# Optimization experiments

Hardware: AMD Instinct MI355X
Metric: run time of the kernel (lower is better)

The kernel has to match this reference:

```python
import jax, jax.numpy as jnp
import numpy as np

N_NODES = 50000
N_EDGES = 600000
IN_DIM = 128
OUT_DIM = 128
EPS = 1e-5


def setup_inputs() -> dict:
    key = jax.random.key(0)
    k1, k2, k3 = jax.random.split(key, 3)
    h = jax.random.normal(k1, (N_NODES, IN_DIM), dtype=jnp.float32)
    edge_index = jax.random.randint(k2, (2, N_EDGES), 0, N_NODES, dtype=jnp.int64)
    ln_gamma = jnp.ones((IN_DIM,), dtype=jnp.float32)
    ln_beta = jnp.zeros((IN_DIM,), dtype=jnp.float32)
    W = jax.random.normal(k3, (OUT_DIM, 2 * IN_DIM), dtype=jnp.float32) * (1.0 / np.sqrt(2 * IN_DIM))
    b = jnp.zeros((OUT_DIM,), dtype=jnp.float32)
    return {"h": h, "edge_index": edge_index, "ln_gamma": ln_gamma,
            "ln_beta": ln_beta, "W": W, "b": b}


def _layernorm(x, gamma, beta):
    mu = jnp.mean(x, axis=-1, keepdims=True)
    var = jnp.mean(jnp.square(x - mu), axis=-1, keepdims=True)
    return (x - mu) * jax.lax.rsqrt(var + EPS) * gamma + beta


def reference(h, edge_index, ln_gamma, ln_beta, W, b):
    src, dst = edge_index[0], edge_index[1]
    n = h.shape[0]
    # LayerNorm
    hn = _layernorm(h, ln_gamma, ln_beta)  # [N, D]
    # Degrees (DGL norm='both' clamps to min 1)
    ones = jnp.ones((src.shape[0],), dtype=h.dtype)
    deg_out = jnp.clip(jax.ops.segment_sum(ones, src, num_segments=n), 1.0)
    deg_in = jnp.clip(jax.ops.segment_sum(ones, dst, num_segments=n), 1.0)
    inv_sqrt_out = jax.lax.rsqrt(deg_out)  # [N]
    inv_sqrt_in = jax.lax.rsqrt(deg_in)    # [N]
    # SpMM: message = D_in^{-1/2} A D_out^{-1/2} hn
    msg_src = hn * inv_sqrt_out[:, None]                 # scale at source
    gathered = msg_src[src]                              # [E, D] irregular gather
    agg = jax.ops.segment_sum(gathered, dst, num_segments=n)  # [N, D]
    message = agg * inv_sqrt_in[:, None]
    # Concat + Linear (dropout is identity in eval)
    cat = jnp.concatenate([hn, message], axis=1)  # [N, 2D]
    return cat @ W.T + b
```

## Files before the change

kernel.cpp:

```cpp
#include <hip/hip_runtime.h>
#include <stdint.h>

#define N_NODES 50000
#define N_EDGES 600000
#define D       128
#define EPS     1e-5f
#define HG      64
#define NWORDS  25000

typedef __attribute__((ext_vector_type(8))) short bf16x8;
typedef __attribute__((ext_vector_type(4))) float f32x4;

__device__ __forceinline__ unsigned short f2bf(float x) {
    unsigned int u = __float_as_uint(x);
    return (unsigned short)((u + 0x7fffu + ((u >> 16) & 1u)) >> 16);
}

__device__ __forceinline__ int load_idx(const void* e, long long i, int is64) {
    return is64 ? (int)((const long long*)e)[i] : ((const int*)e)[i];
}

__device__ __forceinline__ int block_detect64(const unsigned int* eraw, int* sflag) {
    if (threadIdx.x < 64) {
        unsigned long long nz = __ballot(eraw[2 * threadIdx.x + 1] != 0u);
        if (threadIdx.x == 0) *sflag = (nz == 0ull) ? 1 : 0;
    }
    __syncthreads();
    return *sflag;
}

__global__ __launch_bounds__(1024) void hist_kernel(const unsigned int* __restrict__ eraw,
                                                    unsigned int* __restrict__ partials) {
    __shared__ unsigned int lhist[NWORDS];
    __shared__ int sflag;
    int t = threadIdx.x;
    int which = blockIdx.x >= HG;
    int b     = blockIdx.x & (HG - 1);
    for (int i = t; i < NWORDS; i += 1024) lhist[i] = 0u;
    int is64 = block_detect64(eraw, &sflag);
    const int per = N_EDGES / HG;
    int lo = b * per, hi = lo + per;
    long long base = which ? (long long)N_EDGES : 0ll;
    for (int i = lo + t; i < hi; i += 1024) {
        int v = load_idx(eraw, base + i, is64);
        atomicAdd(&lhist[v >> 1], (v & 1) ? (1u << 16) : 1u);
    }
    __syncthreads();
    unsigned int* dst = partials + (size_t)blockIdx.x * NWORDS;
    for (int i = t; i < NWORDS; i += 1024) dst[i] = lhist[i];
}

__global__ __launch_bounds__(256) void deg_reduce(const unsigned int* __restrict__ partials,
                                                  unsigned int* __restrict__ deg_in,
                                                  float* __restrict__ inv_out,
                                                  float* __restrict__ inv_in) {
    int w = blockIdx.x * 256 + threadIdx.x;
    if (w >= NWORDS) return;
    unsigned int o0 = 0, o1 = 0, d0 = 0, d1 = 0;
    for (int b = 0; b < HG; ++b) {
        unsigned int p = partials[(size_t)b * NWORDS + w];
        o0 += p & 0xffffu; o1 += p >> 16;
    }
    for (int b = 0; b < HG; ++b) {
        unsigned int p = partials[(size_t)(HG + b) * NWORDS + w];
        d0 += p & 0xffffu; d1 += p >> 16;
    }
    deg_in[2 * w]     = d0;
    deg_in[2 * w + 1] = d1;
    inv_out[2 * w]     = rsqrtf((float)(o0 > 1u ? o0 : 1u));
    inv_out[2 * w + 1] = rsqrtf((float)(o1 > 1u ? o1 : 1u));
    inv_in[2 * w]      = rsqrtf((float)(d0 > 1u ? d0 : 1u));
    inv_in[2 * w + 1]  = rsqrtf((float)(d1 > 1u ? d1 : 1u));
}

__global__ __launch_bounds__(1024) void scan1(const unsigned int* __restrict__ deg,
                                              unsigned int* __restrict__ row_start,
                                              unsigned int* __restrict__ partials) {
    __shared__ unsigned int wsum[16];
    int t = threadIdx.x, lane = t & 63, w = t >> 6;
    int i = blockIdx.x * 1024 + t;
    unsigned int v = (i < N_NODES) ? deg[i] : 0u;
    unsigned int x = v;
    #pragma unroll
    for (int off = 1; off < 64; off <<= 1) {
        unsigned int y = __shfl_up(x, off, 64);
        if (lane >= off) x += y;
    }
    if (lane == 63) wsum[w] = x;
    __syncthreads();
    if (w == 0) {
        unsigned int s = (lane < 16) ? wsum[lane] : 0u;
        #pragma unroll
        for (int off = 1; off < 16; off <<= 1) {
            unsigned int y = __shfl_up(s, off, 64);
            if (lane >= off) s += y;
        }
        if (lane < 16) wsum[lane] = s;
    }
    __syncthreads();
    unsigned int excl = (w ? wsum[w - 1] : 0u) + x - v;
    if (i < N_NODES) row_start[i] = excl;
    if (t == 1023) partials[blockIdx.x] = wsum[15];
}

__global__ __launch_bounds__(1024) void scan2(const unsigned int* __restrict__ partials,
                                              unsigned int* __restrict__ row_start) {
    __shared__ unsigned int soff;
    int t = threadIdx.x, b = blockIdx.x;
    if (t < 64) {
        unsigned int p = (t < b) ? partials[t] : 0u;
        #pragma unroll
        for (int off = 32; off; off >>= 1) p += __shfl_xor(p, off, 64);
        if (t == 0) soff = p;
    }
    __syncthreads();
    int i = b * 1024 + t;
    if (i < N_NODES) row_start[i] += soff;
    if (b == 0 && t == 0) row_start[N_NODES] = N_EDGES;
}

__global__ __launch_bounds__(256) void prefix_kernel(const unsigned int* __restrict__ partials,
                                                     const unsigned int* __restrict__ row_start,
                                                     unsigned int* __restrict__ pre) {
    int w = blockIdx.x * 256 + threadIdx.x;
    if (w >= NWORDS) return;
    unsigned int run0 = row_start[2 * w], run1 = row_start[2 * w + 1];
    for (int b = 0; b < HG; ++b) {
        pre[(size_t)b * N_NODES + 2 * w]     = run0;
        pre[(size_t)b * N_NODES + 2 * w + 1] = run1;
        unsigned int p = partials[(size_t)(HG + b) * NWORDS + w];
        run0 += p & 0xffffu; run1 += p >> 16;
    }
}

__global__ __launch_bounds__(1024) void fill_kernel(const unsigned int* __restrict__ eraw,
                                                    const unsigned int* __restrict__ pre,
                                                    unsigned int* __restrict__ csr_src) {
    __shared__ unsigned int lcur[NWORDS];
    __shared__ int sflag;
    int t = threadIdx.x, b = blockIdx.x;
    for (int i = t; i < NWORDS; i += 1024) lcur[i] = 0u;
    int is64 = block_detect64(eraw, &sflag);
    const int per = N_EDGES / HG;
    int lo = b * per, hi = lo + per;
    const unsigned int* preb = pre + (size_t)b * N_NODES;
    for (int i = lo + t; i < hi; i += 1024) {
        int s = load_idx(eraw, i, is64);
        int d = load_idx(eraw, (long long)N_EDGES + i, is64);
        unsigned int old = atomicAdd(&lcur[d >> 1], (d & 1) ? (1u << 16) : 1u);
        unsigned int pl = (d & 1) ? (old >> 16) : (old & 0xffffu);
        csr_src[preb[d] + pl] = (unsigned int)s;
    }
}

__global__ __launch_bounds__(256) void ln_kernel(const float2* __restrict__ h2,
                                                 const float2* __restrict__ g2,
                                                 const float2* __restrict__ b2,
                                                 unsigned int* __restrict__ hnb) {
    int wid  = threadIdx.x >> 6;
    int lane = threadIdx.x & 63;
    int row  = blockIdx.x * 4 + wid;
    if (row >= N_NODES) return;
    float2 v = h2[(size_t)row * 64 + lane];
    float s  = v.x + v.y;
    float ss = v.x * v.x + v.y * v.y;
    #pragma unroll
    for (int off = 32; off; off >>= 1) {
        s  += __shfl_xor(s,  off, 64);
        ss += __shfl_xor(ss, off, 64);
    }
    float mu  = s * (1.0f / D);
    float var = ss * (1.0f / D) - mu * mu;
    float rs  = rsqrtf(var + EPS);
    float2 g = g2[lane], b = b2[lane];
    float y0 = (v.x - mu) * rs * g.x + b.x;
    float y1 = (v.y - mu) * rs * g.y + b.y;
    hnb[(size_t)row * 64 + lane] = (unsigned int)f2bf(y0) | ((unsigned int)f2bf(y1) << 16);
}

__global__ __launch_bounds__(256) void cast_W(const float2* __restrict__ W2,
                                              unsigned int* __restrict__ Wb) {
    int i = blockIdx.x * 256 + threadIdx.x;
    if (i < 128 * 128) {
        float2 w = W2[i];
        Wb[i] = (unsigned int)f2bf(w.x) | ((unsigned int)f2bf(w.y) << 16);
    }
}

__global__ __launch_bounds__(256) void agg_kernel(const unsigned int* __restrict__ hnb,
                                                  const float* __restrict__ inv_out,
                                                  const float* __restrict__ inv_in,
                                                  const unsigned int* __restrict__ row_start,
                                                  const unsigned int* __restrict__ csr_src,
                                                  unsigned int* __restrict__ aggb) {
    int wid  = threadIdx.x >> 6;
    int lane = threadIdx.x & 63;
    int row  = blockIdx.x * 4 + wid;
    if (row >= N_NODES) return;
    int g = lane >> 4, gl = lane & 15;
    unsigned int e0 = row_start[row], e1 = row_start[row + 1];
    float acc[8];
    #pragma unroll
    for (int j = 0; j < 8; ++j) acc[j] = 0.0f;

    unsigned int e = e0;
    while (e < e1) {
        unsigned int cnt = e1 - e;
        if (cnt > 64u) cnt = 64u;
        int sl = (lane < (int)cnt) ? (int)csr_src[e + lane] : 0;
        int nit = ((int)cnt + 3) >> 2;
        for (int it = 0; it < nit; ++it) {
            int idx = it * 4 + g;
            int s = __shfl(sl, idx, 64);
            if (idx < (int)cnt) {
                float sc = inv_out[s];
                uint4 v = *(const uint4*)(hnb + (size_t)s * 64 + gl * 4);
                acc[0] = fmaf(__uint_as_float(v.x << 16),          sc, acc[0]);
                acc[1] = fmaf(__uint_as_float(v.x & 0xffff0000u),  sc, acc[1]);
                acc[2] = fmaf(__uint_as_float(v.y << 16),          sc, acc[2]);
                acc[3] = fmaf(__uint_as_float(v.y & 0xffff0000u),  sc, acc[3]);
                acc[4] = fmaf(__uint_as_float(v.z << 16),          sc, acc[4]);
                acc[5] = fmaf(__uint_as_float(v.z & 0xffff0000u),  sc, acc[5]);
                acc[6] = fmaf(__uint_as_float(v.w << 16),          sc, acc[6]);
                acc[7] = fmaf(__uint_as_float(v.w & 0xffff0000u),  sc, acc[7]);
            }
        }
        e += cnt;
    }
    #pragma unroll
    for (int j = 0; j < 8; ++j) {
        acc[j] += __shfl_xor(acc[j], 16, 64);
        acc[j] += __shfl_xor(acc[j], 32, 64);
    }
    if (g == 0) {
        float ii = inv_in[row];
        uint4 o;
        o.x = (unsigned int)f2bf(acc[0] * ii) | ((unsigned int)f2bf(acc[1] * ii) << 16);
        o.y = (unsigned int)f2bf(acc[2] * ii) | ((unsigned int)f2bf(acc[3] * ii) << 16);
        o.z = (unsigned int)f2bf(acc[4] * ii) | ((unsigned int)f2bf(acc[5] * ii) << 16);
        o.w = (unsigned int)f2bf(acc[6] * ii) | ((unsigned int)f2bf(acc[7] * ii) << 16);
        *(uint4*)(aggb + (size_t)row * 64 + gl * 4) = o;
    }
}

__global__ __launch_bounds__(256) void gemm_kernel(const unsigned short* __restrict__ hnb,
                                                   const unsigned short* __restrict__ aggb,
                                                   const unsigned short* __restrict__ Wb,
                                                   const float* __restrict__ bias,
                                                   float* __restrict__ out) {
    __shared__ unsigned short wlds[128 * 264];
    int t = threadIdx.x;
    {
        int j = t >> 1, half = t & 1;
        const uint4* src = (const uint4*)(Wb + (size_t)j * 256 + half * 128);
        uint4* dst = (uint4*)(wlds + j * 264 + half * 128);
        #pragma unroll
        for (int i = 0; i < 16; ++i) dst[i] = src[i];
    }
    __syncthreads();

    int w = t >> 6, lane = t & 63;
    int rbase = blockIdx.x * 64 + w * 16;
    if (rbase >= N_NODES) return;
    int lrow = lane & 15, lhi = lane >> 4;

    bf16x8 a[8];
    const unsigned short* hrow = hnb + (size_t)(rbase + lrow) * 128 + lhi * 8;
    const unsigned short* arow = aggb + (size_t)(rbase + lrow) * 128 + lhi * 8;
    #pragma unroll
    for (int kc = 0; kc < 4; ++kc) a[kc]     = *(const bf16x8*)(hrow + kc * 32);
    #pragma unroll
    for (int kc = 0; kc < 4; ++kc) a[4 + kc] = *(const bf16x8*)(arow + kc * 32);

    f32x4 acc[8];
    #pragma unroll
    for (int ct = 0; ct < 8; ++ct) acc[ct] = (f32x4){0.f, 0.f, 0.f, 0.f};

    #pragma unroll
    for (int ct = 0; ct < 8; ++ct) {
        const unsigned short* bb = wlds + (ct * 16 + lrow) * 264 + lhi * 8;
        #pragma unroll
        for (int kc = 0; kc < 8; ++kc) {
            bf16x8 bfrag = *(const bf16x8*)(bb + kc * 32);
            acc[ct] = __builtin_amdgcn_mfma_f32_16x16x32_bf16(a[kc], bfrag, acc[ct], 0, 0, 0);
        }
    }

    #pragma unroll
    for (int ct = 0; ct < 8; ++ct) {
        int col = ct * 16 + lrow;
        float bv = bias[col];
        #pragma unroll
        for (int i = 0; i < 4; ++i) {
            int row = rbase + lhi * 4 + i;
            out[(size_t)row * 128 + col] = acc[ct][i] + bv;
        }
    }
}

extern "C" void kernel_launch(void* const* d_in, const int* in_sizes, int n_in,
                              void* d_out, int out_size, void* d_ws, size_t ws_size,
                              hipStream_t stream) {
    const float* h     = (const float*)d_in[0];
    const unsigned int* eraw = (const unsigned int*)d_in[1];
    const float* gamma = (const float*)d_in[2];
    const float* beta  = (const float*)d_in[3];
    const float* W     = (const float*)d_in[4];
    const float* bias  = (const float*)d_in[5];
    float* out = (float*)d_out;

    char* ws = (char*)d_ws;
    size_t off = 0;
    auto alloc = [&](size_t bytes) { size_t o = off; off += (bytes + 255) & ~(size_t)255; return o; };
    unsigned int* hpart     = (unsigned int*)(ws + alloc((size_t)2 * HG * NWORDS * 4));
    unsigned int* pre       = (unsigned int*)(ws + alloc((size_t)HG * N_NODES * 4));
    unsigned int* deg_in    = (unsigned int*)(ws + alloc((size_t)N_NODES * 4));
    float*        inv_out   = (float*)(ws + alloc((size_t)N_NODES * 4));
    float*        inv_in    = (float*)(ws + alloc((size_t)N_NODES * 4));
    unsigned int* row_start = (unsigned int*)(ws + alloc((size_t)(N_NODES + 1) * 4));
    unsigned int* spart     = (unsigned int*)(ws + alloc(64 * 4));
    unsigned int* Wb        = (unsigned int*)(ws + alloc((size_t)128 * 256 * 2));
    unsigned int* csr_src   = (unsigned int*)(ws + alloc((size_t)N_EDGES * 4));
    unsigned int* hnb       = (unsigned int*)(ws + alloc((size_t)N_NODES * D * 2));
    unsigned int* aggb      = (unsigned int*)(ws + alloc((size_t)N_NODES * D * 2));

    hist_kernel<<<2 * HG, 1024, 0, stream>>>(eraw, hpart);
    ln_kernel<<<(N_NODES + 3) / 4, 256, 0, stream>>>((const float2*)h, (const float2*)gamma,
                                                     (const float2*)beta, hnb);
    deg_reduce<<<(NWORDS + 255) / 256, 256, 0, stream>>>(hpart, deg_in, inv_out, inv_in);
    scan1<<<(N_NODES + 1023) / 1024, 1024, 0, stream>>>(deg_in, row_start, spart);
    scan2<<<(N_NODES + 1023) / 1024, 1024, 0, stream>>>(spart, row_start);
    prefix_kernel<<<(NWORDS + 255) / 256, 256, 0, stream>>>(hpart, row_start, pre);
    cast_W<<<64, 256, 0, stream>>>((const float2*)W, Wb);
    fill_kernel<<<HG, 1024, 0, stream>>>(eraw, pre, csr_src);
    agg_kernel<<<(N_NODES + 3) / 4, 256, 0, stream>>>(hnb, inv_out, inv_in, row_start,
                                                      csr_src, aggb);
    gemm_kernel<<<(N_NODES + 63) / 64, 256, 0, stream>>>((const unsigned short*)hnb,
                                                         (const unsigned short*)aggb,
                                                         (const unsigned short*)Wb,
                                                         bias, out);
}
```

Measured before the change: 110.1 us.

## Fuse degree reduce into scan, prefix into scan2, W cast into hist; widen agg gather

Merges the degree reduction into the first scan kernel, the per-block prefix computation into the second scan kernel, and the W bf16 cast into the histogram kernel. Together these cut the launch count from ten to seven and drop the deg_in buffer. The aggregation kernel now processes 8 edges per wave iteration, with each lane loading two 16-byte chunks and keeping 16 accumulators, instead of 4 edges per iteration. The fused scan reads partials per node rather than per word, which doubles those reads. The wider aggregation raises register pressure.

```diff
diff --git a/kernel.cpp b/kernel.cpp
--- a/kernel.cpp
+++ b/kernel.cpp
@@ -30,7 +30,9 @@
 }
 
 __global__ __launch_bounds__(1024) void hist_kernel(const unsigned int* __restrict__ eraw,
-                                                    unsigned int* __restrict__ partials) {
+                                                    unsigned int* __restrict__ partials,
+                                                    const float2* __restrict__ W2,
+                                                    unsigned int* __restrict__ Wb) {
     __shared__ unsigned int lhist[NWORDS];
     __shared__ int sflag;
     int t = threadIdx.x;
@@ -48,38 +50,35 @@
     __syncthreads();
     unsigned int* dst = partials + (size_t)blockIdx.x * NWORDS;
     for (int i = t; i < NWORDS; i += 1024) dst[i] = lhist[i];
-}
-
-__global__ __launch_bounds__(256) void deg_reduce(const unsigned int* __restrict__ partials,
-                                                  unsigned int* __restrict__ deg_in,
-                                                  float* __restrict__ inv_out,
-                                                  float* __restrict__ inv_in) {
-    int w = blockIdx.x * 256 + threadIdx.x;
-    if (w >= NWORDS) return;
-    unsigned int o0 = 0, o1 = 0, d0 = 0, d1 = 0;
-    for (int b = 0; b < HG; ++b) {
-        unsigned int p = partials[(size_t)b * NWORDS + w];
-        o0 += p & 0xffffu; o1 += p >> 16;
-    }
-    for (int b = 0; b < HG; ++b) {
-        unsigned int p = partials[(size_t)(HG + b) * NWORDS + w];
-        d0 += p & 0xffffu; d1 += p >> 16;
-    }
-    deg_in[2 * w]     = d0;
-    deg_in[2 * w + 1] = d1;
-    inv_out[2 * w]     = rsqrtf((float)(o0 > 1u ? o0 : 1u));
-    inv_out[2 * w + 1] = rsqrtf((float)(o1 > 1u ? o1 : 1u));
-    inv_in[2 * w]      = rsqrtf((float)(d0 > 1u ? d0 : 1u));
-    inv_in[2 * w + 1]  = rsqrtf((float)(d1 > 1u ? d1 : 1u));
-}
-
-__global__ __launch_bounds__(1024) void scan1(const unsigned int* __restrict__ deg,
-                                              unsigned int* __restrict__ row_start,
-                                              unsigned int* __restrict__ partials) {
+    if (blockIdx.x == 0) {
+        for (int i = t; i < 128 * 128; i += 1024) {
+            float2 w = W2[i];
+            Wb[i] = (unsigned int)f2bf(w.x) | ((unsigned int)f2bf(w.y) << 16);
+        }
+    }
+}
+
+__global__ __launch_bounds__(1024) void scan1r(const unsigned int* __restrict__ partials,
+                                               float* __restrict__ inv_out,
+                                               float* __restrict__ inv_in,
+                                               unsigned int* __restrict__ row_start,
+                                               unsigned int* __restrict__ spart) {
     __shared__ unsigned int wsum[16];
     int t = threadIdx.x, lane = t & 63, w = t >> 6;
     int i = blockIdx.x * 1024 + t;
-    unsigned int v = (i < N_NODES) ? deg[i] : 0u;
+    unsigned int od = 0, dd = 0;
+    if (i < N_NODES) {
+        int word = i >> 1, hi = i & 1;
+        for (int b = 0; b < HG; ++b) {
+            unsigned int ps = partials[(size_t)b * NWORDS + word];
+            unsigned int pd = partials[(size_t)(HG + b) * NWORDS + word];
+            od += hi ? (ps >> 16) : (ps & 0xffffu);
+            dd += hi ? (pd >> 16) : (pd & 0xffffu);
+        }
+        inv_out[i] = rsqrtf((float)(od > 1u ? od : 1u));
+        inv_in[i]  = rsqrtf((float)(dd > 1u ? dd : 1u));
+    }
+    unsigned int v = (i < N_NODES) ? dd : 0u;
     unsigned int x = v;
     #pragma unroll
     for (int off = 1; off < 64; off <<= 1) {
@@ -100,36 +99,40 @@
     __syncthreads();
     unsigned int excl = (w ? wsum[w - 1] : 0u) + x - v;
     if (i < N_NODES) row_start[i] = excl;
-    if (t == 1023) partials[blockIdx.x] = wsum[15];
-}
-
-__global__ __launch_bounds__(1024) void scan2(const unsigned int* __restrict__ partials,
-                                              unsigned int* __restrict__ row_start) {
-    __shared__ unsigned int soff;
+    if (t == 1023) spart[blockIdx.x] = wsum[15];
+}
+
+__global__ __launch_bounds__(1024) void scan2p(const unsigned int* __restrict__ partials,
+                                               const unsigned int* __restrict__ spart,
+                                               unsigned int* __restrict__ row_start,
+                                               unsigned int* __restrict__ pre) {
+    __shared__ unsigned int soff_s;
     int t = threadIdx.x, b = blockIdx.x;
     if (t < 64) {
-        unsigned int p = (t < b) ? partials[t] : 0u;
+        unsigned int p = (t < b) ? spart[t] : 0u;
         #pragma unroll
         for (int off = 32; off; off >>= 1) p += __shfl_xor(p, off, 64);
-        if (t == 0) soff = p;
-    }
-    __syncthreads();
+        if (t == 0) soff_s = p;
+    }
+    __syncthreads();
+    unsigned int soff = soff_s;
     int i = b * 1024 + t;
     if (i < N_NODES) row_start[i] += soff;
     if (b == 0 && t == 0) row_start[N_NODES] = N_EDGES;
-}
-
-__global__ __launch_bounds__(256) void prefix_kernel(const unsigned int* __restrict__ partials,
-                                                     const unsigned int* __restrict__ row_start,
-                                                     unsigned int* __restrict__ pre) {
-    int w = blockIdx.x * 256 + threadIdx.x;
-    if (w >= NWORDS) return;
-    unsigned int run0 = row_start[2 * w], run1 = row_start[2 * w + 1];
-    for (int b = 0; b < HG; ++b) {
-        pre[(size_t)b * N_NODES + 2 * w]     = run0;
-        pre[(size_t)b * N_NODES + 2 * w + 1] = run1;
-        unsigned int p = partials[(size_t)(HG + b) * NWORDS + w];
-        run0 += p & 0xffffu; run1 += p >> 16;
+    __syncthreads();
+    if (t < 512) {
+        int w2 = b * 512 + t;
+        if (w2 < NWORDS) {
+            unsigned int run0 = row_start[2 * w2];
+            unsigned int run1 = row_start[2 * w2 + 1];
+            for (int bb = 0; bb < HG; ++bb) {
+                pre[(size_t)bb * N_NODES + 2 * w2]     = run0;
+                pre[(size_t)bb * N_NODES + 2 * w2 + 1] = run1;
+                unsigned int p = partials[(size_t)(HG + bb) * NWORDS + w2];
+                run0 += p & 0xffffu;
+                run1 += p >> 16;
+            }
+        }
     }
 }
 
@@ -178,15 +181,6 @@
     hnb[(size_t)row * 64 + lane] = (unsigned int)f2bf(y0) | ((unsigned int)f2bf(y1) << 16);
 }
 
-__global__ __launch_bounds__(256) void cast_W(const float2* __restrict__ W2,
-                                              unsigned int* __restrict__ Wb) {
-    int i = blockIdx.x * 256 + threadIdx.x;
-    if (i < 128 * 128) {
-        float2 w = W2[i];
-        Wb[i] = (unsigned int)f2bf(w.x) | ((unsigned int)f2bf(w.y) << 16);
-    }
-}
-
 __global__ __launch_bounds__(256) void agg_kernel(const unsigned int* __restrict__ hnb,
                                                   const float* __restrict__ inv_out,
                                                   const float* __restrict__ inv_in,
@@ -197,49 +191,66 @@
     int lane = threadIdx.x & 63;
     int row  = blockIdx.x * 4 + wid;
     if (row >= N_NODES) return;
-    int g = lane >> 4, gl = lane & 15;
+    int g = lane >> 3, gl = lane & 7;
     unsigned int e0 = row_start[row], e1 = row_start[row + 1];
-    float acc[8];
-    #pragma unroll
-    for (int j = 0; j < 8; ++j) acc[j] = 0.0f;
+    float acc[16];
+    #pragma unroll
+    for (int j = 0; j < 16; ++j) acc[j] = 0.0f;
 
     unsigned int e = e0;
     while (e < e1) {
         unsigned int cnt = e1 - e;
         if (cnt > 64u) cnt = 64u;
         int sl = (lane < (int)cnt) ? (int)csr_src[e + lane] : 0;
-        int nit = ((int)cnt + 3) >> 2;
+        int nit = ((int)cnt + 7) >> 3;
         for (int it = 0; it < nit; ++it) {
-            int idx = it * 4 + g;
+            int idx = it * 8 + g;
             int s = __shfl(sl, idx, 64);
             if (idx < (int)cnt) {
                 float sc = inv_out[s];
-                uint4 v = *(const uint4*)(hnb + (size_t)s * 64 + gl * 4);
-                acc[0] = fmaf(__uint_as_float(v.x << 16),          sc, acc[0]);
-                acc[1] = fmaf(__uint_as_float(v.x & 0xffff0000u),  sc, acc[1]);
-                acc[2] = fmaf(__uint_as_float(v.y << 16),          sc, acc[2]);
-                acc[3] = fmaf(__uint_as_float(v.y & 0xffff0000u),  sc, acc[3]);
-                acc[4] = fmaf(__uint_as_float(v.z << 16),          sc, acc[4]);
-                acc[5] = fmaf(__uint_as_float(v.z & 0xffff0000u),  sc, acc[5]);
-                acc[6] = fmaf(__uint_as_float(v.w << 16),          sc, acc[6]);
-                acc[7] = fmaf(__uint_as_float(v.w & 0xffff0000u),  sc, acc[7]);
+                const uint4* rp = (const uint4*)(hnb + (size_t)s * 64);
+                uint4 vl = rp[gl];
+                uint4 vh = rp[8 + gl];
+                acc[0]  = fmaf(__uint_as_float(vl.x << 16),         sc, acc[0]);
+                acc[1]  = fmaf(__uint_as_float(vl.x & 0xffff0000u), sc, acc[1]);
+                acc[2]  = fmaf(__uint_as_float(vl.y << 16),         sc, acc[2]);
+                acc[3]  = fmaf(__uint_as_float(vl.y & 0xffff0000u), sc, acc[3]);
+                acc[4]  = fmaf(__uint_as_float(vl.z << 16),         sc, acc[4]);
+                acc[5]  = fmaf(__uint_as_float(vl.z & 0xffff0000u), sc, acc[5]);
+                acc[6]  = fmaf(__uint_as_float(vl.w << 16),         sc, acc[6]);
+                acc[7]  = fmaf(__uint_as_float(vl.w & 0xffff0000u), sc, acc[7]);
+                acc[8]  = fmaf(__uint_as_float(vh.x << 16),         sc, acc[8]);
+                acc[9]  = fmaf(__uint_as_float(vh.x & 0xffff0000u), sc, acc[9]);
+                acc[10] = fmaf(__uint_as_float(vh.y << 16),         sc, acc[10]);
+                acc[11] = fmaf(__uint_as_float(vh.y & 0xffff0000u), sc, acc[11]);
+                acc[12] = fmaf(__uint_as_float(vh.z << 16),         sc, acc[12]);
+                acc[13] = fmaf(__uint_as_float(vh.z & 0xffff0000u), sc, acc[13]);
+                acc[14] = fmaf(__uint_as_float(vh.w << 16),         sc, acc[14]);
+                acc[15] = fmaf(__uint_as_float(vh.w & 0xffff0000u), sc, acc[15]);
             }
         }
         e += cnt;
     }
     #pragma unroll
-    for (int j = 0; j < 8; ++j) {
+    for (int j = 0; j < 16; ++j) {
+        acc[j] += __shfl_xor(acc[j], 8, 64);
         acc[j] += __shfl_xor(acc[j], 16, 64);
         acc[j] += __shfl_xor(acc[j], 32, 64);
     }
-    if (g == 0) {
+    if (lane < 8) {
         float ii = inv_in[row];
-        uint4 o;
-        o.x = (unsigned int)f2bf(acc[0] * ii) | ((unsigned int)f2bf(acc[1] * ii) << 16);
-        o.y = (unsigned int)f2bf(acc[2] * ii) | ((unsigned int)f2bf(acc[3] * ii) << 16);
-        o.z = (unsigned int)f2bf(acc[4] * ii) | ((unsigned int)f2bf(acc[5] * ii) << 16);
-        o.w = (unsigned int)f2bf(acc[6] * ii) | ((unsigned int)f2bf(acc[7] * ii) << 16);
-        *(uint4*)(aggb + (size_t)row * 64 + gl * 4) = o;
+        uint4 lo, hi;
+        lo.x = (unsigned int)f2bf(acc[0]  * ii) | ((unsigned int)f2bf(acc[1]  * ii) << 16);
+        lo.y = (unsigned int)f2bf(acc[2]  * ii) | ((unsigned int)f2bf(acc[3]  * ii) << 16);
+        lo.z = (unsigned int)f2bf(acc[4]  * ii) | ((unsigned int)f2bf(acc[5]  * ii) << 16);
+        lo.w = (unsigned int)f2bf(acc[6]  * ii) | ((unsigned int)f2bf(acc[7]  * ii) << 16);
+        hi.x = (unsigned int)f2bf(acc[8]  * ii) | ((unsigned int)f2bf(acc[9]  * ii) << 16);
+        hi.y = (unsigned int)f2bf(acc[10] * ii) | ((unsigned int)f2bf(acc[11] * ii) << 16);
+        hi.z = (unsigned int)f2bf(acc[12] * ii) | ((unsigned int)f2bf(acc[13] * ii) << 16);
+        hi.w = (unsigned int)f2bf(acc[14] * ii) | ((unsigned int)f2bf(acc[15] * ii) << 16);
+        uint4* ap = (uint4*)(aggb + (size_t)row * 64);
+        ap[lane]     = lo;
+        ap[8 + lane] = hi;
     }
 }
 
@@ -314,7 +325,6 @@
     auto alloc = [&](size_t bytes) { size_t o = off; off += (bytes + 255) & ~(size_t)255; return o; };
     unsigned int* hpart     = (unsigned int*)(ws + alloc((size_t)2 * HG * NWORDS * 4));
     unsigned int* pre       = (unsigned int*)(ws + alloc((size_t)HG * N_NODES * 4));
-    unsigned int* deg_in    = (unsigned int*)(ws + alloc((size_t)N_NODES * 4));
     float*        inv_out   = (float*)(ws + alloc((size_t)N_NODES * 4));
     float*        inv_in    = (float*)(ws + alloc((size_t)N_NODES * 4));
     unsigned int* row_start = (unsigned int*)(ws + alloc((size_t)(N_NODES + 1) * 4));
@@ -324,14 +334,12 @@
     unsigned int* hnb       = (unsigned int*)(ws + alloc((size_t)N_NODES * D * 2));
     unsigned int* aggb      = (unsigned int*)(ws + alloc((size_t)N_NODES * D * 2));
 
-    hist_kernel<<<2 * HG, 1024, 0, stream>>>(eraw, hpart);
+    hist_kernel<<<2 * HG, 1024, 0, stream>>>(eraw, hpart, (const float2*)W, Wb);
     ln_kernel<<<(N_NODES + 3) / 4, 256, 0, stream>>>((const float2*)h, (const float2*)gamma,
                                                      (const float2*)beta, hnb);
-    deg_reduce<<<(NWORDS + 255) / 256, 256, 0, stream>>>(hpart, deg_in, inv_out, inv_in);
-    scan1<<<(N_NODES + 1023) / 1024, 1024, 0, stream>>>(deg_in, row_start, spart);
-    scan2<<<(N_NODES + 1023) / 1024, 1024, 0, stream>>>(spart, row_start);
-    prefix_kernel<<<(NWORDS + 255) / 256, 256, 0, stream>>>(hpart, row_start, pre);
-    cast_W<<<64, 256, 0, stream>>>((const float2*)W, Wb);
+    scan1r<<<(N_NODES + 1023) / 1024, 1024, 0, stream>>>(hpart, inv_out, inv_in,
+                                                         row_start, spart);
+    scan2p<<<(N_NODES + 1023) / 1024, 1024, 0, stream>>>(hpart, spart, row_start, pre);
     fill_kernel<<<HG, 1024, 0, stream>>>(eraw, pre, csr_src);
     agg_kernel<<<(N_NODES + 3) / 4, 256, 0, stream>>>(hnb, inv_out, inv_in, row_start,
                                                       csr_src, aggb);
```

Result: slower. 115.5 us (+5.0%).
